# Performance work log

Measured on AMD Instinct MI355X. Metric: run time of the kernel, lower is better.

Reference implementation:

```python
import jax, jax.numpy as jnp
import numpy as np
from jax import lax

KERNEL = 3
K = 3


def setup_inputs() -> dict:
    key = jax.random.key(0)
    xcorr = jax.random.normal(key, (16, 1, 256, 8192), dtype=jnp.float32)
    return {"xcorr": xcorr}


def reference(xcorr):
    # xcorr: [B, C, H, W] (W = lag axis)
    W = xcorr.shape[-1]
    nlag = W // 2
    # max_pool2d with kernel (1,KERNEL), stride 1, padding (0, KERNEL//2).
    # torch pads with -inf for max pooling.
    neg_inf = jnp.asarray(-jnp.inf, dtype=xcorr.dtype)
    pad = KERNEL // 2
    smax = lax.reduce_window(
        xcorr,
        neg_inf,
        lax.max,
        window_dimensions=(1, 1, 1, KERNEL),
        window_strides=(1, 1, 1, 1),
        padding=[(0, 0), (0, 0), (0, 0), (pad, pad)],
    )
    keep = (smax == xcorr).astype(xcorr.dtype)  # local-max NMS mask
    scores = xcorr * keep
    topk_scores, topk_inds = lax.top_k(scores, K)  # sorted descending, [B,C,H,K]
    top = topk_inds[..., 0]  # best peak index [B,C,H]
    nearby = jnp.clip(
        jnp.stack([top - 1, top, top + 1], axis=-1), 0, W - 1
    )  # [B,C,H,3]
    neighbor_score = jnp.take_along_axis(xcorr, nearby, axis=-1)
    topk_index = topk_inds - nlag
    return neighbor_score, topk_scores, topk_index
```

## Files before the change

### kernel.cpp

```cpp
#include <hip/hip_runtime.h>
#include <climits>
#include <cmath>


#define PW    8192
#define PNLAG (PW / 2)
#define BLOCK 256
#define NW    4
#define J     8

typedef __attribute__((address_space(1))) const void global_cv;
typedef __attribute__((address_space(3))) void lds_v;

__device__ __forceinline__ bool better(float av, int ai, float bv, int bi) {
  return (av > bv) || ((av == bv) && (ai < bi));
}

__device__ __forceinline__ void insert3_full(float v, int i,
                                             float &v0, int &i0,
                                             float &v1, int &i1,
                                             float &v2, int &i2) {
  if (better(v, i, v2, i2)) {
    if (better(v, i, v1, i1)) {
      if (better(v, i, v0, i0)) {
        v2 = v1; i2 = i1; v1 = v0; i1 = i0; v0 = v; i0 = i;
      } else {
        v2 = v1; i2 = i1; v1 = v; i1 = i;
      }
    } else {
      v2 = v; i2 = i;
    }
  }
}

__device__ __forceinline__ void insert3_fast(float c, int ci,
                                             float &v0, int &i0,
                                             float &v1, int &i1,
                                             float &v2, int &i2) {
  const bool b2 = c > v2;
  const bool b1 = c > v1;
  const bool b0 = c > v0;
  v2 = b1 ? v1 : (b2 ? c : v2);  i2 = b1 ? i1 : (b2 ? ci : i2);
  v1 = b0 ? v0 : (b1 ? c : v1);  i1 = b0 ? i0 : (b1 ? ci : i1);
  v0 = b0 ? c  : v0;             i0 = b0 ? ci : i0;
}

__global__ __launch_bounds__(BLOCK)
void detect_peaks_kernel(const float* __restrict__ x,
                         float* __restrict__ out,
                         int rows) {
  __shared__ float sx[PW];
  __shared__ float rv[12];
  __shared__ int   ri[12];

  const int row  = blockIdx.x;
  const int t    = threadIdx.x;
  const int lane = t & 63;
  const int wave = t >> 6;
  const float* __restrict__ xr = x + (size_t)row * PW;

  const int waveQ = wave * (J * 64);

#pragma unroll
  for (int j = 0; j < J; ++j) {
    const float* gsrc = xr + (size_t)(waveQ + j * 64 + lane) * 4;
    float*       ldst = sx + (size_t)(waveQ + j * 64) * 4;
    __builtin_amdgcn_global_load_lds((global_cv*)gsrc, (lds_v*)ldst, 16, 0, 0);
  }
  __syncthreads();

  float v0 = -INFINITY, v1 = -INFINITY, v2 = -INFINITY;
  int   i0 = INT_MAX,   i1 = INT_MAX,   i2 = INT_MAX;

#pragma unroll
  for (int j = 0; j < J; ++j) {
    const int p = (waveQ + j * 64 + lane) * 4;
    const float4 v = *(const float4*)(sx + p);

    const int   li = (p == 0) ? 0 : p - 1;
    const float left  = (p == 0)      ? -INFINITY : sx[li];
    const int   riq = (p + 4 >= PW) ? PW - 1 : p + 4;
    const float right = (p + 4 >= PW) ? -INFINITY : sx[riq];

    const float p01 = fmaxf(v.x, v.y);
    const float p12 = fmaxf(v.y, v.z);
    const float p23 = fmaxf(v.z, v.w);
    const float m0 = fmaxf(left, p01);
    const float m1 = fmaxf(p01, v.z);
    const float m2 = fmaxf(p12, v.w);
    const float m3 = fmaxf(p23, right);

    const float s0 = (v.x == m0) ? v.x : 0.0f;
    const float s1 = (v.y == m1) ? v.y : 0.0f;
    const float s2 = (v.z == m2) ? v.z : 0.0f;
    const float s3 = (v.w == m3) ? v.w : 0.0f;

    const bool  a01 = s0 >= s1;
    const float hiA = a01 ? s0 : s1;   const int hiAi = a01 ? p     : p + 1;
    const float loA = a01 ? s1 : s0;   const int loAi = a01 ? p + 1 : p;
    const bool  a23 = s2 >= s3;
    const float hiB = a23 ? s2 : s3;   const int hiBi = a23 ? p + 2 : p + 3;
    const float loB = a23 ? s3 : s2;   const int loBi = a23 ? p + 3 : p + 2;

    const bool  ab  = hiA >= hiB;
    const float c1  = ab ? hiA : hiB;  const int c1i = ab ? hiAi : hiBi;
    const bool  sb  = ab ? (loA >= hiB) : (hiA >= loB);
    const float c2  = ab ? (sb ? loA : hiB) : (sb ? hiA : loB);
    const int   c2i = ab ? (sb ? loAi : hiBi) : (sb ? hiAi : loBi);

    insert3_fast(c1, c1i, v0, i0, v1, i1, v2, i2);
    insert3_fast(c2, c2i, v0, i0, v1, i1, v2, i2);
  }

#pragma unroll
  for (int off = 32; off > 0; off >>= 1) {
    float ov0 = __shfl_down(v0, off);
    int   oi0 = __shfl_down(i0, off);
    float ov1 = __shfl_down(v1, off);
    int   oi1 = __shfl_down(i1, off);
    float ov2 = __shfl_down(v2, off);
    int   oi2 = __shfl_down(i2, off);
    if (lane + off < 64) {
      insert3_full(ov0, oi0, v0, i0, v1, i1, v2, i2);
      insert3_full(ov1, oi1, v0, i0, v1, i1, v2, i2);
      insert3_full(ov2, oi2, v0, i0, v1, i1, v2, i2);
    }
  }

  if (lane == 0) {
    rv[wave * 3 + 0] = v0; ri[wave * 3 + 0] = i0;
    rv[wave * 3 + 1] = v1; ri[wave * 3 + 1] = i1;
    rv[wave * 3 + 2] = v2; ri[wave * 3 + 2] = i2;
  }
  __syncthreads();

  if (t == 0) {
#pragma unroll
    for (int w = 1; w < NW; ++w) {
      insert3_full(rv[w * 3 + 0], ri[w * 3 + 0], v0, i0, v1, i1, v2, i2);
      insert3_full(rv[w * 3 + 1], ri[w * 3 + 1], v0, i0, v1, i1, v2, i2);
      insert3_full(rv[w * 3 + 2], ri[w * 3 + 2], v0, i0, v1, i1, v2, i2);
    }

    float* __restrict__ nb = out;
    float* __restrict__ ts = out + (size_t)rows * 3;
    float* __restrict__ ti = out + (size_t)rows * 6;

    const int top = i0;
#pragma unroll
    for (int k = 0; k < 3; ++k) {
      int idx = top - 1 + k;
      idx = idx < 0 ? 0 : (idx > PW - 1 ? PW - 1 : idx);
      nb[row * 3 + k] = sx[idx];
    }
    ts[row * 3 + 0] = v0;
    ts[row * 3 + 1] = v1;
    ts[row * 3 + 2] = v2;
    ti[row * 3 + 0] = (float)(i0 - PNLAG);
    ti[row * 3 + 1] = (float)(i1 - PNLAG);
    ti[row * 3 + 2] = (float)(i2 - PNLAG);
  }
}

extern "C" void kernel_launch(void* const* d_in, const int* in_sizes, int n_in,
                              void* d_out, int out_size, void* d_ws, size_t ws_size,
                              hipStream_t stream) {
  const float* x = (const float*)d_in[0];
  float* out = (float*)d_out;
  const int rows = in_sizes[0] / PW;
  detect_peaks_kernel<<<rows, BLOCK, 0, stream>>>(x, out, rows);
}
```

Before: 233.7 us.

## Replace LDS row staging with register streaming and wave shuffles for neighbors

Drops the 32KB shared-memory staging of each row. Each wave now streams its own contiguous span straight from global memory into registers with one-step prefetch, and gets the left and right neighbors through lane shuffles plus a carry across iterations. Only two edge elements per wave are read separately. This removes the block-wide barrier and the LDS footprint, which allows more resident blocks (launch bounds hint 8), at the cost of extra shuffle instructions and a final neighbor-score gather from global memory.

```diff
diff --git a/kernel.cpp b/kernel.cpp
--- a/kernel.cpp
+++ b/kernel.cpp
@@ -8,9 +8,6 @@
 #define BLOCK 256
 #define NW    4
 #define J     8
-
-typedef __attribute__((address_space(1))) const void global_cv;
-typedef __attribute__((address_space(3))) void lds_v;
 
 __device__ __forceinline__ bool better(float av, int ai, float bv, int bi) {
   return (av > bv) || ((av == bv) && (ai < bi));
@@ -45,13 +42,12 @@
   v0 = b0 ? c  : v0;             i0 = b0 ? ci : i0;
 }
 
-__global__ __launch_bounds__(BLOCK)
+__global__ __launch_bounds__(BLOCK, 8)
 void detect_peaks_kernel(const float* __restrict__ x,
                          float* __restrict__ out,
                          int rows) {
-  __shared__ float sx[PW];
-  __shared__ float rv[12];
-  __shared__ int   ri[12];
+  __shared__ float rv[NW * 3];
+  __shared__ int   ri[NW * 3];
 
   const int row  = blockIdx.x;
   const int t    = threadIdx.x;
@@ -59,41 +55,45 @@
   const int wave = t >> 6;
   const float* __restrict__ xr = x + (size_t)row * PW;
 
-  const int waveQ = wave * (J * 64);
+  const int span = J * 64 * 4;
+  const int base = wave * span;
 
-#pragma unroll
-  for (int j = 0; j < J; ++j) {
-    const float* gsrc = xr + (size_t)(waveQ + j * 64 + lane) * 4;
-    float*       ldst = sx + (size_t)(waveQ + j * 64) * 4;
-    __builtin_amdgcn_global_load_lds((global_cv*)gsrc, (lds_v*)ldst, 16, 0, 0);
-  }
-  __syncthreads();
+  const float edgeL = (base > 0)         ? xr[base - 1]    : -INFINITY;
+  const float edgeR = (base + span < PW) ? xr[base + span] : -INFINITY;
 
   float v0 = -INFINITY, v1 = -INFINITY, v2 = -INFINITY;
   int   i0 = INT_MAX,   i1 = INT_MAX,   i2 = INT_MAX;
 
+  float4 cur = *(const float4*)(xr + base + lane * 4);
+  float carry = edgeL;
+
 #pragma unroll
   for (int j = 0; j < J; ++j) {
-    const int p = (waveQ + j * 64 + lane) * 4;
-    const float4 v = *(const float4*)(sx + p);
+    float4 nxt = cur;
+    if (j + 1 < J)
+      nxt = *(const float4*)(xr + base + ((j + 1) * 64 + lane) * 4);
 
-    const int   li = (p == 0) ? 0 : p - 1;
-    const float left  = (p == 0)      ? -INFINITY : sx[li];
-    const int   riq = (p + 4 >= PW) ? PW - 1 : p + 4;
-    const float right = (p + 4 >= PW) ? -INFINITY : sx[riq];
+    float left = __shfl_up(cur.w, 1);
+    if (lane == 0) left = carry;
+    const float nfirst = (j + 1 < J) ? __shfl(nxt.x, 0) : edgeR;
+    float right = __shfl_down(cur.x, 1);
+    if (lane == 63) right = nfirst;
+    carry = __shfl(cur.w, 63);
 
-    const float p01 = fmaxf(v.x, v.y);
-    const float p12 = fmaxf(v.y, v.z);
-    const float p23 = fmaxf(v.z, v.w);
+    const int p = base + (j * 64 + lane) * 4;
+
+    const float p01 = fmaxf(cur.x, cur.y);
+    const float p12 = fmaxf(cur.y, cur.z);
+    const float p23 = fmaxf(cur.z, cur.w);
     const float m0 = fmaxf(left, p01);
-    const float m1 = fmaxf(p01, v.z);
-    const float m2 = fmaxf(p12, v.w);
+    const float m1 = fmaxf(p01, cur.z);
+    const float m2 = fmaxf(p12, cur.w);
     const float m3 = fmaxf(p23, right);
 
-    const float s0 = (v.x == m0) ? v.x : 0.0f;
-    const float s1 = (v.y == m1) ? v.y : 0.0f;
-    const float s2 = (v.z == m2) ? v.z : 0.0f;
-    const float s3 = (v.w == m3) ? v.w : 0.0f;
+    const float s0 = (cur.x == m0) ? cur.x : 0.0f;
+    const float s1 = (cur.y == m1) ? cur.y : 0.0f;
+    const float s2 = (cur.z == m2) ? cur.z : 0.0f;
+    const float s3 = (cur.w == m3) ? cur.w : 0.0f;
 
     const bool  a01 = s0 >= s1;
     const float hiA = a01 ? s0 : s1;   const int hiAi = a01 ? p     : p + 1;
@@ -110,6 +110,8 @@
 
     insert3_fast(c1, c1i, v0, i0, v1, i1, v2, i2);
     insert3_fast(c2, c2i, v0, i0, v1, i1, v2, i2);
+
+    cur = nxt;
   }
 
 #pragma unroll
@@ -151,7 +153,7 @@
     for (int k = 0; k < 3; ++k) {
       int idx = top - 1 + k;
       idx = idx < 0 ? 0 : (idx > PW - 1 ? PW - 1 : idx);
-      nb[row * 3 + k] = sx[idx];
+      nb[row * 3 + k] = xr[idx];
     }
     ts[row * 3 + 0] = v0;
     ts[row * 3 + 1] = v1;
```

New measurement: 241.5 us. 1.03x slower.

## Replace LDS staging with register loads and cross-lane shuffles for neighbors

Applied to the files above, without the earlier changes.

Drops the 32KB shared-memory row buffer and the async global-to-LDS loads. Each thread now loads its float4 chunks straight into registers, and each chunk's left and right neighbors come from wave shuffles, with two scalar loads covering the boundaries between waves. Freeing the LDS, together with a launch-bounds occupancy hint, is meant to let more blocks share a CU and hide memory latency. The cost is extra shuffle instructions and more register pressure, and the final neighbor gather now re-reads global memory.

```diff
diff --git a/kernel.cpp b/kernel.cpp
--- a/kernel.cpp
+++ b/kernel.cpp
@@ -8,9 +8,6 @@
 #define BLOCK 256
 #define NW    4
 #define J     8
-
-typedef __attribute__((address_space(1))) const void global_cv;
-typedef __attribute__((address_space(3))) void lds_v;
 
 __device__ __forceinline__ bool better(float av, int ai, float bv, int bi) {
   return (av > bv) || ((av == bv) && (ai < bi));
@@ -45,13 +42,12 @@
   v0 = b0 ? c  : v0;             i0 = b0 ? ci : i0;
 }
 
-__global__ __launch_bounds__(BLOCK)
+__global__ __launch_bounds__(BLOCK, 4)
 void detect_peaks_kernel(const float* __restrict__ x,
                          float* __restrict__ out,
                          int rows) {
-  __shared__ float sx[PW];
-  __shared__ float rv[12];
-  __shared__ int   ri[12];
+  __shared__ float rv[NW * 3];
+  __shared__ int   ri[NW * 3];
 
   const int row  = blockIdx.x;
   const int t    = threadIdx.x;
@@ -59,28 +55,32 @@
   const int wave = t >> 6;
   const float* __restrict__ xr = x + (size_t)row * PW;
 
-  const int waveQ = wave * (J * 64);
+  const int span = J * 64 * 4;
+  const int base = wave * span;
 
+  float4 q[J];
 #pragma unroll
-  for (int j = 0; j < J; ++j) {
-    const float* gsrc = xr + (size_t)(waveQ + j * 64 + lane) * 4;
-    float*       ldst = sx + (size_t)(waveQ + j * 64) * 4;
-    __builtin_amdgcn_global_load_lds((global_cv*)gsrc, (lds_v*)ldst, 16, 0, 0);
-  }
-  __syncthreads();
+  for (int j = 0; j < J; ++j)
+    q[j] = *(const float4*)(xr + base + (j * 64 + lane) * 4);
+
+  const float edgeL = (base > 0)         ? xr[base - 1]    : -INFINITY;
+  const float edgeR = (base + span < PW) ? xr[base + span] : -INFINITY;
 
   float v0 = -INFINITY, v1 = -INFINITY, v2 = -INFINITY;
   int   i0 = INT_MAX,   i1 = INT_MAX,   i2 = INT_MAX;
 
 #pragma unroll
   for (int j = 0; j < J; ++j) {
-    const int p = (waveQ + j * 64 + lane) * 4;
-    const float4 v = *(const float4*)(sx + p);
+    const float4 v = q[j];
 
-    const int   li = (p == 0) ? 0 : p - 1;
-    const float left  = (p == 0)      ? -INFINITY : sx[li];
-    const int   riq = (p + 4 >= PW) ? PW - 1 : p + 4;
-    const float right = (p + 4 >= PW) ? -INFINITY : sx[riq];
+    float left = __shfl_up(v.w, 1);
+    const float lf = (j == 0) ? edgeL : __shfl(q[j - 1].w, 63);
+    if (lane == 0) left = lf;
+    float right = __shfl_down(v.x, 1);
+    const float rf = (j == J - 1) ? edgeR : __shfl(q[j + 1].x, 0);
+    if (lane == 63) right = rf;
+
+    const int p = base + (j * 64 + lane) * 4;
 
     const float p01 = fmaxf(v.x, v.y);
     const float p12 = fmaxf(v.y, v.z);
@@ -151,7 +151,7 @@
     for (int k = 0; k < 3; ++k) {
       int idx = top - 1 + k;
       idx = idx < 0 ? 0 : (idx > PW - 1 ? PW - 1 : idx);
-      nb[row * 3 + k] = sx[idx];
+      nb[row * 3 + k] = xr[idx];
     }
     ts[row * 3 + 0] = v0;
     ts[row * 3 + 1] = v1;
```

After: 240.5 us. +2.9%, slower.

## Pipeline per-wave LDS loads with vmcnt waits and shuffle-based neighbors

Applied to the files above, without the earlier changes.

Each wave now owns a contiguous 2048-element span of the row and fetches its own halo edges directly from global memory. This lets the block-wide barrier after the async global-to-LDS loads be replaced by per-segment s_waitcnt vmcnt waits, so compute on early segments overlaps with later loads still in flight. Left and right neighbors now come from wave shuffles rather than extra LDS reads, and only the boundary lanes touch LDS or the edge values. The code relies on the in-order vmcnt accounting covering the LDS writes of the async loads, so a miscounted wait would read stale data.

```diff
diff --git a/kernel.cpp b/kernel.cpp
--- a/kernel.cpp
+++ b/kernel.cpp
@@ -7,10 +7,12 @@
 #define PNLAG (PW / 2)
 #define BLOCK 256
 #define NW    4
-#define J     8
+#define SEGS  8
 
 typedef __attribute__((address_space(1))) const void global_cv;
 typedef __attribute__((address_space(3))) void lds_v;
+
+#define WAIT_VM(n) asm volatile("s_waitcnt vmcnt(" #n ")" ::: "memory")
 
 __device__ __forceinline__ bool better(float av, int ai, float bv, int bi) {
   return (av > bv) || ((av == bv) && (ai < bi));
@@ -50,8 +52,8 @@
                          float* __restrict__ out,
                          int rows) {
   __shared__ float sx[PW];
-  __shared__ float rv[12];
-  __shared__ int   ri[12];
+  __shared__ float rv[NW * 3];
+  __shared__ int   ri[NW * 3];
 
   const int row  = blockIdx.x;
   const int t    = threadIdx.x;
@@ -59,28 +61,43 @@
   const int wave = t >> 6;
   const float* __restrict__ xr = x + (size_t)row * PW;
 
-  const int waveQ = wave * (J * 64);
+  const int W = wave * 2048;
+
+  const float edgeL = (W > 0)         ? xr[W - 1]    : -INFINITY;
+  const float edgeR = (W + 2048 < PW) ? xr[W + 2048] : -INFINITY;
+  __builtin_amdgcn_sched_barrier(0);
 
 #pragma unroll
-  for (int j = 0; j < J; ++j) {
-    const float* gsrc = xr + (size_t)(waveQ + j * 64 + lane) * 4;
-    float*       ldst = sx + (size_t)(waveQ + j * 64) * 4;
+  for (int s = 0; s < SEGS; ++s) {
+    const float* gsrc = xr + (size_t)(W + s * 256 + lane * 4);
+    float*       ldst = sx + (size_t)(W + s * 256);
     __builtin_amdgcn_global_load_lds((global_cv*)gsrc, (lds_v*)ldst, 16, 0, 0);
   }
-  __syncthreads();
+  __builtin_amdgcn_sched_barrier(0);
 
   float v0 = -INFINITY, v1 = -INFINITY, v2 = -INFINITY;
   int   i0 = INT_MAX,   i1 = INT_MAX,   i2 = INT_MAX;
 
 #pragma unroll
-  for (int j = 0; j < J; ++j) {
-    const int p = (waveQ + j * 64 + lane) * 4;
+  for (int s = 0; s < SEGS; ++s) {
+    switch (s) {
+      case 0: WAIT_VM(6); break;
+      case 1: WAIT_VM(5); break;
+      case 2: WAIT_VM(4); break;
+      case 3: WAIT_VM(3); break;
+      case 4: WAIT_VM(2); break;
+      case 5: WAIT_VM(1); break;
+      default: WAIT_VM(0); break;
+    }
+
+    const int segbase = W + s * 256;
+    const int p = segbase + lane * 4;
     const float4 v = *(const float4*)(sx + p);
 
-    const int   li = (p == 0) ? 0 : p - 1;
-    const float left  = (p == 0)      ? -INFINITY : sx[li];
-    const int   riq = (p + 4 >= PW) ? PW - 1 : p + 4;
-    const float right = (p + 4 >= PW) ? -INFINITY : sx[riq];
+    float left = __shfl_up(v.w, 1);
+    if (lane == 0) left = (s == 0) ? edgeL : sx[segbase - 1];
+    float right = __shfl_down(v.x, 1);
+    if (lane == 63) right = (s == SEGS - 1) ? edgeR : sx[segbase + 256];
 
     const float p01 = fmaxf(v.x, v.y);
     const float p12 = fmaxf(v.y, v.z);
```

Measured after the change: 234.5 us. No clear change (+0.3%).
